# Optimization experiments

Measured on AMD Instinct MI355X. Metric: run time of the kernel, lower is better.

## Reference

```python
import jax, jax.numpy as jnp
import numpy as np

N = 50000   # query points
N2 = 50000  # key/value points
C = 128     # n_channels
G = 8       # n_groups
S = 16      # n_samples
CS = C // G # n_share_channels
EPS = 1e-5


def setup_inputs() -> dict:
    key = jax.random.key(0)
    ks = jax.random.split(key, 16)
    std = 0.02
    return {
        "p": jax.random.normal(ks[0], (N, 3), jnp.float32),
        "x": jax.random.normal(ks[1], (N, C), jnp.float32),
        "p2": jax.random.normal(ks[2], (N2, 3), jnp.float32),
        "x2": jax.random.normal(ks[3], (N2, C), jnp.float32),
        "idx": jax.random.randint(ks[4], (N, S), 0, N2, jnp.int32),
        "Wq": jax.random.normal(ks[5], (C, C), jnp.float32) * std,
        "bq": jnp.zeros((C,), jnp.float32),
        "Wk": jax.random.normal(ks[6], (C, C), jnp.float32) * std,
        "bk": jnp.zeros((C,), jnp.float32),
        "Wv": jax.random.normal(ks[7], (C, C), jnp.float32) * std,
        "bv": jnp.zeros((C,), jnp.float32),
        # linear_p: Conv1d(3,3,1) -> BN(3) -> ReLU -> Conv1d(3, 2G, 1)
        "W1": jax.random.normal(ks[8], (3, 3), jnp.float32) * 0.5,
        "b1": jnp.zeros((3,), jnp.float32),
        "bn_gamma": jnp.ones((3,), jnp.float32),
        "bn_beta": jnp.zeros((3,), jnp.float32),
        "bn_mean": jnp.zeros((3,), jnp.float32),
        "bn_var": jnp.ones((3,), jnp.float32),
        "W2": jax.random.normal(ks[9], (2 * G, 3), jnp.float32) * 0.5,
        "b2": jnp.zeros((2 * G,), jnp.float32),
    }


def reference(p, x, p2, x2, idx,
              Wq, bq, Wk, bk, Wv, bv,
              W1, b1, bn_gamma, bn_beta, bn_mean, bn_var, W2, b2):
    n = x.shape[0]
    # Q/K/V projections
    x_q = x @ Wq.T + bq                       # (n, C)
    x_k = (x2 @ Wk.T + bk)[idx]               # (n, S, C)  KNN gather
    x_v = (x2 @ Wv.T + bv)[idx]               # (n, S, C)
    # relative positions
    p_r = p2[idx] - p[:, None, :]             # (n, S, 3)
    # linear_p (pointwise convs == per-neighbor MLP over the 3 coord channels)
    h = p_r @ W1.T + b1
    h = (h - bn_mean) * jax.lax.rsqrt(bn_var + EPS) * bn_gamma + bn_beta
    h = jax.nn.relu(h)
    pe = h @ W2.T + b2                        # (n, S, 2G)
    p_rq, p_rk = jnp.split(pe, 2, axis=-1)    # each (n, S, G)
    # grouped attention
    k4 = x_k.reshape(n, S, G, CS) + p_rk[..., None]
    q4 = x_q.reshape(n, 1, G, CS) + p_rq[..., None]
    logits = jnp.sum(k4 * q4, axis=-1) / np.float32(np.sqrt(CS))  # (n, S, G)
    w = jax.nn.softmax(logits, axis=1)        # softmax over neighbors
    out = jnp.einsum('nsgc,nsg->ngc', x_v.reshape(n, S, G, CS), w)
    return out.reshape(n, C)
```

## Files before the change

kernel.cpp:

```cpp
#include <hip/hip_runtime.h>
#include <hip/hip_bf16.h>

#define NQ   50000
#define NKV  50000
#define CC   128
#define GG   8
#define SS   16
#define CSH  16

typedef short    bf16x8 __attribute__((ext_vector_type(8)));
typedef float    f32x4  __attribute__((ext_vector_type(4)));
typedef unsigned u32x4  __attribute__((ext_vector_type(4)));
typedef unsigned u32x2  __attribute__((ext_vector_type(2)));
typedef int      i32x4  __attribute__((ext_vector_type(4)));

__device__ __forceinline__ float bf_lo(unsigned u){ union{unsigned x; float f;} v; v.x = u << 16;        return v.f; }
__device__ __forceinline__ float bf_hi(unsigned u){ union{unsigned x; float f;} v; v.x = u & 0xffff0000u; return v.f; }
__device__ __forceinline__ unsigned short f2bfu(float f){
    __hip_bfloat16 h = __float2bfloat16(f);
    return *reinterpret_cast<unsigned short*>(&h);
}
__device__ __forceinline__ short f2bfs(float f){
    __hip_bfloat16 h = __float2bfloat16(f);
    return *reinterpret_cast<short*>(&h);
}

__device__ __forceinline__ void load16bf(const __hip_bfloat16* ptr, float* o){
    const u32x4* p4 = reinterpret_cast<const u32x4*>(ptr);
    u32x4 a = p4[0]; u32x4 b = p4[1];
    o[0]=bf_lo(a[0]);  o[1]=bf_hi(a[0]);  o[2]=bf_lo(a[1]);  o[3]=bf_hi(a[1]);
    o[4]=bf_lo(a[2]);  o[5]=bf_hi(a[2]);  o[6]=bf_lo(a[3]);  o[7]=bf_hi(a[3]);
    o[8]=bf_lo(b[0]);  o[9]=bf_hi(b[0]);  o[10]=bf_lo(b[1]); o[11]=bf_hi(b[1]);
    o[12]=bf_lo(b[2]); o[13]=bf_hi(b[2]); o[14]=bf_lo(b[3]); o[15]=bf_hi(b[3]);
}

__device__ __forceinline__ bf16x8 cvt8(const float* p){
    const f32x4* q = reinterpret_cast<const f32x4*>(p);
    f32x4 u = q[0], v = q[1];
    bf16x8 r;
    r[0]=f2bfs(u[0]); r[1]=f2bfs(u[1]); r[2]=f2bfs(u[2]); r[3]=f2bfs(u[3]);
    r[4]=f2bfs(v[0]); r[5]=f2bfs(v[1]); r[6]=f2bfs(v[2]); r[7]=f2bfs(v[3]);
    return r;
}

__global__ __launch_bounds__(256) void qkv_gemm(
    const float* __restrict__ x,
    const float* __restrict__ x2,
    const float* __restrict__ Wq, const float* __restrict__ Wk,
    const float* __restrict__ Wv,
    const float* __restrict__ bq, const float* __restrict__ bk,
    const float* __restrict__ bv,
    __hip_bfloat16* __restrict__ Qf,
    __hip_bfloat16* __restrict__ KVf)
{
    __shared__ short lds16[16384];

    const int tid  = threadIdx.x;
    const int wave = tid >> 6;
    const int lane = tid & 63;
    const int r    = lane & 15;
    const int kq   = lane >> 4;
    const int base = blockIdx.x * 128 + wave * 32;

    auto stageW = [&](const float* __restrict__ W){
        #pragma unroll
        for (int i = 0; i < 8; ++i) {
            const int o   = i * 2048 + tid * 8;
            const bf16x8 v = cvt8(W + o);
            const int row = o >> 7, col = o & 127;
            const int lchunk = (((row >> 4) * 4 + (col >> 5)) << 6)
                             + (((col >> 3) & 3) << 4) + (row & 15);
            *reinterpret_cast<bf16x8*>(&lds16[lchunk * 8]) = v;
        }
    };

    auto loadB = [&](const float* __restrict__ src, bf16x8 (&bfrag)[2][4]){
        #pragma unroll
        for (int mt = 0; mt < 2; ++mt) {
            int row = base + mt * 16 + r;
            if (row >= NQ) row = NQ - 1;
            const float* xr = src + (size_t)row * CC + kq * 8;
            #pragma unroll
            for (int kb = 0; kb < 4; ++kb)
                bfrag[mt][kb] = cvt8(xr + kb * 32);
        }
    };

    auto runTiles = [&](const bf16x8 (&bfrag)[2][4], const float* __restrict__ bias,
                        short* __restrict__ dstb, int dstride, int hoff){
        #pragma unroll
        for (int t = 0; t < 8; ++t) {
            bf16x8 af[4];
            #pragma unroll
            for (int kb = 0; kb < 4; ++kb)
                af[kb] = *reinterpret_cast<const bf16x8*>(
                    &lds16[(((t * 4 + kb) << 6) + lane) * 8]);

            f32x4 acc0 = {0.f,0.f,0.f,0.f}, acc1 = {0.f,0.f,0.f,0.f};
            #pragma unroll
            for (int kb = 0; kb < 4; ++kb) {
                acc0 = __builtin_amdgcn_mfma_f32_16x16x32_bf16(af[kb], bfrag[0][kb], acc0, 0, 0, 0);
                acc1 = __builtin_amdgcn_mfma_f32_16x16x32_bf16(af[kb], bfrag[1][kb], acc1, 0, 0, 0);
            }

            const f32x4 bi = *reinterpret_cast<const f32x4*>(bias + t * 16 + kq * 4);
            #pragma unroll
            for (int mt = 0; mt < 2; ++mt) {
                const int row = base + mt * 16 + r;
                if (row < NQ) {
                    const f32x4 a = mt ? acc1 : acc0;
                    u32x2 pk;
                    pk[0] = (unsigned)f2bfu(a[0] + bi[0]) | ((unsigned)f2bfu(a[1] + bi[1]) << 16);
                    pk[1] = (unsigned)f2bfu(a[2] + bi[2]) | ((unsigned)f2bfu(a[3] + bi[3]) << 16);
                    *reinterpret_cast<u32x2*>(
                        dstb + (size_t)row * dstride + hoff + t * 16 + kq * 4) = pk;
                }
            }
        }
    };

    bf16x8 fq[2][4], fkv[2][4];
    loadB(x,  fq);
    loadB(x2, fkv);

    stageW(Wq);
    __syncthreads();
    runTiles(fq, bq, (short*)Qf, CC, 0);
    __syncthreads();
    stageW(Wk);
    __syncthreads();
    runTiles(fkv, bk, (short*)KVf, 2 * CC, 0);
    __syncthreads();
    stageW(Wv);
    __syncthreads();
    runTiles(fkv, bv, (short*)KVf, 2 * CC, CC);
}

__global__ __launch_bounds__(256) void attn_kernel(
    const float* __restrict__ p,
    const float* __restrict__ p2,
    const int*   __restrict__ idx,
    const float* __restrict__ W1,
    const float* __restrict__ b1,
    const float* __restrict__ bn_gamma,
    const float* __restrict__ bn_beta,
    const float* __restrict__ bn_mean,
    const float* __restrict__ bn_var,
    const float* __restrict__ W2,
    const float* __restrict__ b2,
    const __hip_bfloat16* __restrict__ Qf,
    const __hip_bfloat16* __restrict__ KVf,
    float* __restrict__ out)
{
    const int tid = blockIdx.x * 256 + threadIdx.x;
    if (tid >= NQ * GG) return;
    const int n = tid >> 3;
    const int g = tid & 7;

    float fw1[3][3], fb1[3];
    #pragma unroll
    for (int j = 0; j < 3; ++j) {
        const float sc = bn_gamma[j] * rsqrtf(bn_var[j] + 1e-5f);
        #pragma unroll
        for (int k = 0; k < 3; ++k) fw1[j][k] = W1[j*3 + k] * sc;
        fb1[j] = (b1[j] - bn_mean[j]) * sc + bn_beta[j];
    }
    const float w2q0 = W2[g*3+0],     w2q1 = W2[g*3+1],     w2q2 = W2[g*3+2];
    const float w2k0 = W2[(g+8)*3+0], w2k1 = W2[(g+8)*3+1], w2k2 = W2[(g+8)*3+2];
    const float b2q = b2[g], b2k = b2[g+8];

    const float px = p[(size_t)n*3+0];
    const float py = p[(size_t)n*3+1];
    const float pz = p[(size_t)n*3+2];

    int nbr[SS];
    {
        const i32x4* ip = reinterpret_cast<const i32x4*>(idx + (size_t)n * SS);
        i32x4 i0 = ip[0], i1 = ip[1], i2 = ip[2], i3 = ip[3];
        nbr[0]=i0[0]; nbr[1]=i0[1]; nbr[2]=i0[2]; nbr[3]=i0[3];
        nbr[4]=i1[0]; nbr[5]=i1[1]; nbr[6]=i1[2]; nbr[7]=i1[3];
        nbr[8]=i2[0]; nbr[9]=i2[1]; nbr[10]=i2[2]; nbr[11]=i2[3];
        nbr[12]=i3[0]; nbr[13]=i3[1]; nbr[14]=i3[2]; nbr[15]=i3[3];
    }

    float q[CSH];
    load16bf(Qf + (size_t)n * CC + g * CSH, q);

    float acc[CSH];
    #pragma unroll
    for (int c = 0; c < CSH; ++c) acc[c] = 0.f;
    float sum = 0.f;
    float m = -3.0e38f;

    #pragma unroll 4
    for (int s = 0; s < SS; ++s) {
        const int i = nbr[s];
        const __hip_bfloat16* kv = KVf + (size_t)i * (2 * CC) + g * CSH;

        float kk[CSH], vv[CSH];
        load16bf(kv, kk);
        load16bf(kv + CC, vv);

        const float rx = p2[(size_t)i*3+0] - px;
        const float ry = p2[(size_t)i*3+1] - py;
        const float rz = p2[(size_t)i*3+2] - pz;
        const float h0 = fmaxf(fw1[0][0]*rx + fw1[0][1]*ry + fw1[0][2]*rz + fb1[0], 0.f);
        const float h1 = fmaxf(fw1[1][0]*rx + fw1[1][1]*ry + fw1[1][2]*rz + fb1[1], 0.f);
        const float h2 = fmaxf(fw1[2][0]*rx + fw1[2][1]*ry + fw1[2][2]*rz + fb1[2], 0.f);
        const float prq = w2q0*h0 + w2q1*h1 + w2q2*h2 + b2q;
        const float prk = w2k0*h0 + w2k1*h1 + w2k2*h2 + b2k;

        float d = 0.f;
        #pragma unroll
        for (int c = 0; c < CSH; ++c) d += (kk[c] + prk) * (q[c] + prq);
        d *= 0.25f;

        const float mnew = fmaxf(m, d);
        const float corr = __expf(m - mnew);
        const float w    = __expf(d - mnew);
        sum = sum * corr + w;
        #pragma unroll
        for (int c = 0; c < CSH; ++c) acc[c] = acc[c] * corr + w * vv[c];
        m = mnew;
    }

    const float inv = 1.f / sum;

    f32x4* op = reinterpret_cast<f32x4*>(out + (size_t)n * CC + g * CSH);
    f32x4 o0 = {acc[0]*inv,  acc[1]*inv,  acc[2]*inv,  acc[3]*inv};
    f32x4 o1 = {acc[4]*inv,  acc[5]*inv,  acc[6]*inv,  acc[7]*inv};
    f32x4 o2 = {acc[8]*inv,  acc[9]*inv,  acc[10]*inv, acc[11]*inv};
    f32x4 o3 = {acc[12]*inv, acc[13]*inv, acc[14]*inv, acc[15]*inv};
    op[0] = o0; op[1] = o1; op[2] = o2; op[3] = o3;
}

extern "C" void kernel_launch(void* const* d_in, const int* in_sizes, int n_in,
                              void* d_out, int out_size, void* d_ws, size_t ws_size,
                              hipStream_t stream) {
    const float* p   = (const float*)d_in[0];
    const float* x   = (const float*)d_in[1];
    const float* p2  = (const float*)d_in[2];
    const float* x2  = (const float*)d_in[3];
    const int*   idx = (const int*)d_in[4];
    const float* Wq  = (const float*)d_in[5];
    const float* bq  = (const float*)d_in[6];
    const float* Wk  = (const float*)d_in[7];
    const float* bk  = (const float*)d_in[8];
    const float* Wv  = (const float*)d_in[9];
    const float* bv  = (const float*)d_in[10];
    const float* W1  = (const float*)d_in[11];
    const float* b1  = (const float*)d_in[12];
    const float* bng = (const float*)d_in[13];
    const float* bnb = (const float*)d_in[14];
    const float* bnm = (const float*)d_in[15];
    const float* bnv = (const float*)d_in[16];
    const float* W2  = (const float*)d_in[17];
    const float* b2  = (const float*)d_in[18];
    float* out = (float*)d_out;

    __hip_bfloat16* Qf  = (__hip_bfloat16*)d_ws;
    __hip_bfloat16* KVf = Qf + (size_t)NQ * CC;

    qkv_gemm<<<dim3(391), 256, 0, stream>>>(
        x, x2, Wq, Wk, Wv, bq, bk, bv, Qf, KVf);

    const int nthreads = NQ * GG;
    attn_kernel<<<(nthreads + 255) / 256, 256, 0, stream>>>(
        p, p2, idx, W1, b1, bng, bnb, bnm, bnv, W2, b2, Qf, KVf, out);
}
```

Before: 212.6 us.

## Split QKV GEMM across grid.y and use two-pass softmax with algebraic dot expansion

The QKV projection kernel now launches a 391x3 grid, one projection per blockIdx.y, so it no longer serialises three weight stagings and tile passes inside each block. This adds parallelism at the cost of loading x2 twice. The attention kernel drops the online softmax. It first computes all 16 logits, expanding (k+prk)·(q+prq) into dot + prq*sumk + prk*sumq + 16*prk*prq, then does a max/exp/normalise pass, then gathers V in a separate loop. This removes the per-step rescaling of the accumulator, but raises register pressure and splits the K and V gathers into two phases.

```diff
diff --git a/kernel.cpp b/kernel.cpp
--- a/kernel.cpp
+++ b/kernel.cpp
@@ -61,79 +61,66 @@
     const int r    = lane & 15;
     const int kq   = lane >> 4;
     const int base = blockIdx.x * 128 + wave * 32;
-
-    auto stageW = [&](const float* __restrict__ W){
-        #pragma unroll
-        for (int i = 0; i < 8; ++i) {
-            const int o   = i * 2048 + tid * 8;
-            const bf16x8 v = cvt8(W + o);
-            const int row = o >> 7, col = o & 127;
-            const int lchunk = (((row >> 4) * 4 + (col >> 5)) << 6)
-                             + (((col >> 3) & 3) << 4) + (row & 15);
-            *reinterpret_cast<bf16x8*>(&lds16[lchunk * 8]) = v;
+    const int proj = blockIdx.y;
+
+    const float* src  = (proj == 0) ? x  : x2;
+    const float* W    = (proj == 0) ? Wq : (proj == 1 ? Wk : Wv);
+    const float* bias = (proj == 0) ? bq : (proj == 1 ? bk : bv);
+    short* dstb   = (proj == 0) ? (short*)Qf : (short*)KVf;
+    const int dstride = (proj == 0) ? CC : 2 * CC;
+    const int hoff    = (proj == 2) ? CC : 0;
+
+    bf16x8 bfrag[2][4];
+    #pragma unroll
+    for (int mt = 0; mt < 2; ++mt) {
+        int row = base + mt * 16 + r;
+        if (row >= NQ) row = NQ - 1;
+        const float* xr = src + (size_t)row * CC + kq * 8;
+        #pragma unroll
+        for (int kb = 0; kb < 4; ++kb)
+            bfrag[mt][kb] = cvt8(xr + kb * 32);
+    }
+
+    #pragma unroll
+    for (int i = 0; i < 8; ++i) {
+        const int o   = i * 2048 + tid * 8;
+        const bf16x8 v = cvt8(W + o);
+        const int row = o >> 7, col = o & 127;
+        const int lchunk = (((row >> 4) * 4 + (col >> 5)) << 6)
+                         + (((col >> 3) & 3) << 4) + (row & 15);
+        *reinterpret_cast<bf16x8*>(&lds16[lchunk * 8]) = v;
+    }
+    __syncthreads();
+
+    #pragma unroll
+    for (int t = 0; t < 8; ++t) {
+        bf16x8 af[4];
+        #pragma unroll
+        for (int kb = 0; kb < 4; ++kb)
+            af[kb] = *reinterpret_cast<const bf16x8*>(
+                &lds16[(((t * 4 + kb) << 6) + lane) * 8]);
+
+        f32x4 acc0 = {0.f,0.f,0.f,0.f}, acc1 = {0.f,0.f,0.f,0.f};
+        #pragma unroll
+        for (int kb = 0; kb < 4; ++kb) {
+            acc0 = __builtin_amdgcn_mfma_f32_16x16x32_bf16(af[kb], bfrag[0][kb], acc0, 0, 0, 0);
+            acc1 = __builtin_amdgcn_mfma_f32_16x16x32_bf16(af[kb], bfrag[1][kb], acc1, 0, 0, 0);
         }
-    };
-
-    auto loadB = [&](const float* __restrict__ src, bf16x8 (&bfrag)[2][4]){
+
+        const f32x4 bi = *reinterpret_cast<const f32x4*>(bias + t * 16 + kq * 4);
         #pragma unroll
         for (int mt = 0; mt < 2; ++mt) {
-            int row = base + mt * 16 + r;
-            if (row >= NQ) row = NQ - 1;
-            const float* xr = src + (size_t)row * CC + kq * 8;
-            #pragma unroll
-            for (int kb = 0; kb < 4; ++kb)
-                bfrag[mt][kb] = cvt8(xr + kb * 32);
-        }
-    };
-
-    auto runTiles = [&](const bf16x8 (&bfrag)[2][4], const float* __restrict__ bias,
-                        short* __restrict__ dstb, int dstride, int hoff){
-        #pragma unroll
-        for (int t = 0; t < 8; ++t) {
-            bf16x8 af[4];
-            #pragma unroll
-            for (int kb = 0; kb < 4; ++kb)
-                af[kb] = *reinterpret_cast<const bf16x8*>(
-                    &lds16[(((t * 4 + kb) << 6) + lane) * 8]);
-
-            f32x4 acc0 = {0.f,0.f,0.f,0.f}, acc1 = {0.f,0.f,0.f,0.f};
-            #pragma unroll
-            for (int kb = 0; kb < 4; ++kb) {
-                acc0 = __builtin_amdgcn_mfma_f32_16x16x32_bf16(af[kb], bfrag[0][kb], acc0, 0, 0, 0);
-                acc1 = __builtin_amdgcn_mfma_f32_16x16x32_bf16(af[kb], bfrag[1][kb], acc1, 0, 0, 0);
-            }
-
-            const f32x4 bi = *reinterpret_cast<const f32x4*>(bias + t * 16 + kq * 4);
-            #pragma unroll
-            for (int mt = 0; mt < 2; ++mt) {
-                const int row = base + mt * 16 + r;
-                if (row < NQ) {
-                    const f32x4 a = mt ? acc1 : acc0;
-                    u32x2 pk;
-                    pk[0] = (unsigned)f2bfu(a[0] + bi[0]) | ((unsigned)f2bfu(a[1] + bi[1]) << 16);
-                    pk[1] = (unsigned)f2bfu(a[2] + bi[2]) | ((unsigned)f2bfu(a[3] + bi[3]) << 16);
-                    *reinterpret_cast<u32x2*>(
-                        dstb + (size_t)row * dstride + hoff + t * 16 + kq * 4) = pk;
-                }
+            const int row = base + mt * 16 + r;
+            if (row < NQ) {
+                const f32x4 a = mt ? acc1 : acc0;
+                u32x2 pk;
+                pk[0] = (unsigned)f2bfu(a[0] + bi[0]) | ((unsigned)f2bfu(a[1] + bi[1]) << 16);
+                pk[1] = (unsigned)f2bfu(a[2] + bi[2]) | ((unsigned)f2bfu(a[3] + bi[3]) << 16);
+                *reinterpret_cast<u32x2*>(
+                    dstb + (size_t)row * dstride + hoff + t * 16 + kq * 4) = pk;
             }
         }
-    };
-
-    bf16x8 fq[2][4], fkv[2][4];
-    loadB(x,  fq);
-    loadB(x2, fkv);
-
-    stageW(Wq);
-    __syncthreads();
-    runTiles(fq, bq, (short*)Qf, CC, 0);
-    __syncthreads();
-    stageW(Wk);
-    __syncthreads();
-    runTiles(fkv, bk, (short*)KVf, 2 * CC, 0);
-    __syncthreads();
-    stageW(Wv);
-    __syncthreads();
-    runTiles(fkv, bv, (short*)KVf, 2 * CC, CC);
+    }
 }
 
 __global__ __launch_bounds__(256) void attn_kernel(
@@ -185,21 +172,16 @@
 
     float q[CSH];
     load16bf(Qf + (size_t)n * CC + g * CSH, q);
-
-    float acc[CSH];
-    #pragma unroll
-    for (int c = 0; c < CSH; ++c) acc[c] = 0.f;
-    float sum = 0.f;
-    float m = -3.0e38f;
-
-    #pragma unroll 4
+    float sumq = 0.f;
+    #pragma unroll
+    for (int c = 0; c < CSH; ++c) sumq += q[c];
+
+    float d[SS];
+    #pragma unroll
     for (int s = 0; s < SS; ++s) {
         const int i = nbr[s];
-        const __hip_bfloat16* kv = KVf + (size_t)i * (2 * CC) + g * CSH;
-
-        float kk[CSH], vv[CSH];
-        load16bf(kv, kk);
-        load16bf(kv + CC, vv);
+        float kk[CSH];
+        load16bf(KVf + (size_t)i * (2 * CC) + g * CSH, kk);
 
         const float rx = p2[(size_t)i*3+0] - px;
         const float ry = p2[(size_t)i*3+1] - py;
@@ -210,27 +192,39 @@
         const float prq = w2q0*h0 + w2q1*h1 + w2q2*h2 + b2q;
         const float prk = w2k0*h0 + w2k1*h1 + w2k2*h2 + b2k;
 
-        float d = 0.f;
-        #pragma unroll
-        for (int c = 0; c < CSH; ++c) d += (kk[c] + prk) * (q[c] + prq);
-        d *= 0.25f;
-
-        const float mnew = fmaxf(m, d);
-        const float corr = __expf(m - mnew);
-        const float w    = __expf(d - mnew);
-        sum = sum * corr + w;
-        #pragma unroll
-        for (int c = 0; c < CSH; ++c) acc[c] = acc[c] * corr + w * vv[c];
-        m = mnew;
-    }
-
+        float dot = 0.f, sumk = 0.f;
+        #pragma unroll
+        for (int c = 0; c < CSH; ++c) { dot += kk[c]*q[c]; sumk += kk[c]; }
+        d[s] = (dot + prq*sumk + prk*sumq + 16.f*prk*prq) * 0.25f;
+    }
+
+    float m = d[0];
+    #pragma unroll
+    for (int s = 1; s < SS; ++s) m = fmaxf(m, d[s]);
+    float w[SS], sum = 0.f;
+    #pragma unroll
+    for (int s = 0; s < SS; ++s) { w[s] = __expf(d[s] - m); sum += w[s]; }
     const float inv = 1.f / sum;
+    #pragma unroll
+    for (int s = 0; s < SS; ++s) w[s] *= inv;
+
+    float acc[CSH];
+    #pragma unroll
+    for (int c = 0; c < CSH; ++c) acc[c] = 0.f;
+    #pragma unroll
+    for (int s = 0; s < SS; ++s) {
+        const int i = nbr[s];
+        float vv[CSH];
+        load16bf(KVf + (size_t)i * (2 * CC) + CC + g * CSH, vv);
+        #pragma unroll
+        for (int c = 0; c < CSH; ++c) acc[c] += w[s] * vv[c];
+    }
 
     f32x4* op = reinterpret_cast<f32x4*>(out + (size_t)n * CC + g * CSH);
-    f32x4 o0 = {acc[0]*inv,  acc[1]*inv,  acc[2]*inv,  acc[3]*inv};
-    f32x4 o1 = {acc[4]*inv,  acc[5]*inv,  acc[6]*inv,  acc[7]*inv};
-    f32x4 o2 = {acc[8]*inv,  acc[9]*inv,  acc[10]*inv, acc[11]*inv};
-    f32x4 o3 = {acc[12]*inv, acc[13]*inv, acc[14]*inv, acc[15]*inv};
+    f32x4 o0 = {acc[0],  acc[1],  acc[2],  acc[3]};
+    f32x4 o1 = {acc[4],  acc[5],  acc[6],  acc[7]};
+    f32x4 o2 = {acc[8],  acc[9],  acc[10], acc[11]};
+    f32x4 o3 = {acc[12], acc[13], acc[14], acc[15]};
     op[0] = o0; op[1] = o1; op[2] = o2; op[3] = o3;
 }
 
@@ -261,7 +255,7 @@
     __hip_bfloat16* Qf  = (__hip_bfloat16*)d_ws;
     __hip_bfloat16* KVf = Qf + (size_t)NQ * CC;
 
-    qkv_gemm<<<dim3(391), 256, 0, stream>>>(
+    qkv_gemm<<<dim3(391, 3), 256, 0, stream>>>(
         x, x2, Wq, Wk, Wv, bq, bk, bv, Qf, KVf);
 
     const int nthreads = NQ * GG;
```

Result: slower. 227.5 us (+7.0%).

## Pre-convert QKV weights to bf16 LDS layout and split projections across grid

Applied to the files above, without the earlier changes.

A small prep kernel now converts Wq/Wk/Wv to bf16 once, already in the LDS tile order. The GEMM kernel takes a second grid dimension so each block handles one projection, and copies its weight tile with global_load_lds direct-to-LDS loads. This removes the repeated per-block fp32-to-bf16 weight conversion and the serialized stage/sync phases, and triples the block count for more parallelism. The cost is an extra kernel launch, and x2 rows are read twice, once by the K block and once by the V block.

```diff
diff --git a/kernel.cpp b/kernel.cpp
--- a/kernel.cpp
+++ b/kernel.cpp
@@ -43,11 +43,30 @@
     return r;
 }
 
+__global__ __launch_bounds__(256) void wprep(
+    const float* __restrict__ Wq, const float* __restrict__ Wk,
+    const float* __restrict__ Wv,
+    __hip_bfloat16* __restrict__ Wp)
+{
+    const float* W = (blockIdx.x == 0) ? Wq : (blockIdx.x == 1) ? Wk : Wv;
+    __hip_bfloat16* o = Wp + blockIdx.x * 16384;
+    #pragma unroll
+    for (int k = 0; k < 8; ++k) {
+        const int chunk = k * 256 + threadIdx.x;
+        const int q   = chunk >> 6;
+        const int rem = chunk & 63;
+        const int c3  = rem >> 4, r15 = rem & 15;
+        const int row  = ((q >> 2) << 4) | r15;
+        const int colb = ((q & 3) << 5) | (c3 << 3);
+        const bf16x8 v = cvt8(W + row * 128 + colb);
+        *reinterpret_cast<bf16x8*>(o + chunk * 8) = v;
+    }
+}
+
 __global__ __launch_bounds__(256) void qkv_gemm(
     const float* __restrict__ x,
     const float* __restrict__ x2,
-    const float* __restrict__ Wq, const float* __restrict__ Wk,
-    const float* __restrict__ Wv,
+    const __hip_bfloat16* __restrict__ Wp,
     const float* __restrict__ bq, const float* __restrict__ bk,
     const float* __restrict__ bv,
     __hip_bfloat16* __restrict__ Qf,
@@ -61,79 +80,67 @@
     const int r    = lane & 15;
     const int kq   = lane >> 4;
     const int base = blockIdx.x * 128 + wave * 32;
-
-    auto stageW = [&](const float* __restrict__ W){
+    const int proj = blockIdx.y;
+
+    const float* src  = (proj == 0) ? x  : x2;
+    const float* bias = (proj == 0) ? bq : (proj == 1 ? bk : bv);
+    short* dstb   = (proj == 0) ? (short*)Qf : (short*)KVf;
+    const int dstride = (proj == 0) ? CC : 2 * CC;
+    const int hoff    = (proj == 2) ? CC : 0;
+
+    {
+        const __hip_bfloat16* Wsrc = Wp + proj * 16384;
         #pragma unroll
         for (int i = 0; i < 8; ++i) {
-            const int o   = i * 2048 + tid * 8;
-            const bf16x8 v = cvt8(W + o);
-            const int row = o >> 7, col = o & 127;
-            const int lchunk = (((row >> 4) * 4 + (col >> 5)) << 6)
-                             + (((col >> 3) & 3) << 4) + (row & 15);
-            *reinterpret_cast<bf16x8*>(&lds16[lchunk * 8]) = v;
+            const int el = i * 2048 + wave * 512;
+            __builtin_amdgcn_global_load_lds(
+                (const __attribute__((address_space(1))) void*)(Wsrc + el + lane * 8),
+                (__attribute__((address_space(3))) void*)(&lds16[el]),
+                16, 0, 0);
         }
-    };
-
-    auto loadB = [&](const float* __restrict__ src, bf16x8 (&bfrag)[2][4]){
+    }
+
+    bf16x8 bfrag[2][4];
+    #pragma unroll
+    for (int mt = 0; mt < 2; ++mt) {
+        int row = base + mt * 16 + r;
+        if (row >= NQ) row = NQ - 1;
+        const float* xr = src + (size_t)row * CC + kq * 8;
+        #pragma unroll
+        for (int kb = 0; kb < 4; ++kb)
+            bfrag[mt][kb] = cvt8(xr + kb * 32);
+    }
+    __syncthreads();
+
+    #pragma unroll
+    for (int t = 0; t < 8; ++t) {
+        bf16x8 af[4];
+        #pragma unroll
+        for (int kb = 0; kb < 4; ++kb)
+            af[kb] = *reinterpret_cast<const bf16x8*>(
+                &lds16[(((t * 4 + kb) << 6) + lane) * 8]);
+
+        f32x4 acc0 = {0.f,0.f,0.f,0.f}, acc1 = {0.f,0.f,0.f,0.f};
+        #pragma unroll
+        for (int kb = 0; kb < 4; ++kb) {
+            acc0 = __builtin_amdgcn_mfma_f32_16x16x32_bf16(af[kb], bfrag[0][kb], acc0, 0, 0, 0);
+            acc1 = __builtin_amdgcn_mfma_f32_16x16x32_bf16(af[kb], bfrag[1][kb], acc1, 0, 0, 0);
+        }
+
+        const f32x4 bi = *reinterpret_cast<const f32x4*>(bias + t * 16 + kq * 4);
         #pragma unroll
         for (int mt = 0; mt < 2; ++mt) {
-            int row = base + mt * 16 + r;
-            if (row >= NQ) row = NQ - 1;
-            const float* xr = src + (size_t)row * CC + kq * 8;
-            #pragma unroll
-            for (int kb = 0; kb < 4; ++kb)
-                bfrag[mt][kb] = cvt8(xr + kb * 32);
-        }
-    };
-
-    auto runTiles = [&](const bf16x8 (&bfrag)[2][4], const float* __restrict__ bias,
-                        short* __restrict__ dstb, int dstride, int hoff){
-        #pragma unroll
-        for (int t = 0; t < 8; ++t) {
-            bf16x8 af[4];
-            #pragma unroll
-            for (int kb = 0; kb < 4; ++kb)
-                af[kb] = *reinterpret_cast<const bf16x8*>(
-                    &lds16[(((t * 4 + kb) << 6) + lane) * 8]);
-
-            f32x4 acc0 = {0.f,0.f,0.f,0.f}, acc1 = {0.f,0.f,0.f,0.f};
-            #pragma unroll
-            for (int kb = 0; kb < 4; ++kb) {
-                acc0 = __builtin_amdgcn_mfma_f32_16x16x32_bf16(af[kb], bfrag[0][kb], acc0, 0, 0, 0);
-                acc1 = __builtin_amdgcn_mfma_f32_16x16x32_bf16(af[kb], bfrag[1][kb], acc1, 0, 0, 0);
-            }
-
-            const f32x4 bi = *reinterpret_cast<const f32x4*>(bias + t * 16 + kq * 4);
-            #pragma unroll
-            for (int mt = 0; mt < 2; ++mt) {
-                const int row = base + mt * 16 + r;
-                if (row < NQ) {
-                    const f32x4 a = mt ? acc1 : acc0;
-                    u32x2 pk;
-                    pk[0] = (unsigned)f2bfu(a[0] + bi[0]) | ((unsigned)f2bfu(a[1] + bi[1]) << 16);
-                    pk[1] = (unsigned)f2bfu(a[2] + bi[2]) | ((unsigned)f2bfu(a[3] + bi[3]) << 16);
-                    *reinterpret_cast<u32x2*>(
-                        dstb + (size_t)row * dstride + hoff + t * 16 + kq * 4) = pk;
-                }
+            const int row = base + mt * 16 + r;
+            if (row < NQ) {
+                const f32x4 a = mt ? acc1 : acc0;
+                u32x2 pk;
+                pk[0] = (unsigned)f2bfu(a[0] + bi[0]) | ((unsigned)f2bfu(a[1] + bi[1]) << 16);
+                pk[1] = (unsigned)f2bfu(a[2] + bi[2]) | ((unsigned)f2bfu(a[3] + bi[3]) << 16);
+                *reinterpret_cast<u32x2*>(
+                    dstb + (size_t)row * dstride + hoff + t * 16 + kq * 4) = pk;
             }
         }
-    };
-
-    bf16x8 fq[2][4], fkv[2][4];
-    loadB(x,  fq);
-    loadB(x2, fkv);
-
-    stageW(Wq);
-    __syncthreads();
-    runTiles(fq, bq, (short*)Qf, CC, 0);
-    __syncthreads();
-    stageW(Wk);
-    __syncthreads();
-    runTiles(fkv, bk, (short*)KVf, 2 * CC, 0);
-    __syncthreads();
-    stageW(Wv);
-    __syncthreads();
-    runTiles(fkv, bv, (short*)KVf, 2 * CC, CC);
+    }
 }
 
 __global__ __launch_bounds__(256) void attn_kernel(
@@ -258,13 +265,15 @@
     const float* b2  = (const float*)d_in[18];
     float* out = (float*)d_out;
 
-    __hip_bfloat16* Qf  = (__hip_bfloat16*)d_ws;
+    __hip_bfloat16* Wp  = (__hip_bfloat16*)d_ws;
+    __hip_bfloat16* Qf  = Wp + 3 * 16384;
     __hip_bfloat16* KVf = Qf + (size_t)NQ * CC;
 
-    qkv_gemm<<<dim3(391), 256, 0, stream>>>(
-        x, x2, Wq, Wk, Wv, bq, bk, bv, Qf, KVf);
-
-    const int nthreads = NQ * GG;
-    attn_kernel<<<(nthreads + 255) / 256, 256, 0, stream>>>(
+    wprep<<<3, 256, 0, stream>>>(Wq, Wk, Wv, Wp);
+
+    qkv_gemm<<<dim3(391, 3), 256, 0, stream>>>(
+        x, x2, Wp, bq, bk, bv, Qf, KVf);
+
+    attn_kernel<<<(NQ * GG + 255) / 256, 256, 0, stream>>>(
         p, p2, idx, W1, b1, bng, bnb, bnm, bnv, W2, b2, Qf, KVf, out);
 }
```

New measurement: 211.0 us. About the same (-0.8%).

## Split QKV projection across a second grid dimension, one projection per block

Applied to the files above, without the earlier changes.

The QKV GEMM kernel now launches a 391x3 grid where blockIdx.y selects the Q, K or V projection, instead of each block computing all three in sequence. This removes the serialized stage-weight/sync/compute phases inside one block and gives three times as many blocks to fill the 256 CUs. The cost is that the x2 tile is loaded and converted twice (once each for the K and V blocks), which adds redundant global reads.

```diff
diff --git a/kernel.cpp b/kernel.cpp
--- a/kernel.cpp
+++ b/kernel.cpp
@@ -61,79 +61,66 @@
     const int r    = lane & 15;
     const int kq   = lane >> 4;
     const int base = blockIdx.x * 128 + wave * 32;
-
-    auto stageW = [&](const float* __restrict__ W){
-        #pragma unroll
-        for (int i = 0; i < 8; ++i) {
-            const int o   = i * 2048 + tid * 8;
-            const bf16x8 v = cvt8(W + o);
-            const int row = o >> 7, col = o & 127;
-            const int lchunk = (((row >> 4) * 4 + (col >> 5)) << 6)
-                             + (((col >> 3) & 3) << 4) + (row & 15);
-            *reinterpret_cast<bf16x8*>(&lds16[lchunk * 8]) = v;
+    const int proj = blockIdx.y;
+
+    const float* src  = (proj == 0) ? x  : x2;
+    const float* W    = (proj == 0) ? Wq : (proj == 1 ? Wk : Wv);
+    const float* bias = (proj == 0) ? bq : (proj == 1 ? bk : bv);
+    short* dstb   = (proj == 0) ? (short*)Qf : (short*)KVf;
+    const int dstride = (proj == 0) ? CC : 2 * CC;
+    const int hoff    = (proj == 2) ? CC : 0;
+
+    bf16x8 bfrag[2][4];
+    #pragma unroll
+    for (int mt = 0; mt < 2; ++mt) {
+        int row = base + mt * 16 + r;
+        if (row >= NQ) row = NQ - 1;
+        const float* xr = src + (size_t)row * CC + kq * 8;
+        #pragma unroll
+        for (int kb = 0; kb < 4; ++kb)
+            bfrag[mt][kb] = cvt8(xr + kb * 32);
+    }
+
+    #pragma unroll
+    for (int i = 0; i < 8; ++i) {
+        const int o   = i * 2048 + tid * 8;
+        const bf16x8 v = cvt8(W + o);
+        const int row = o >> 7, col = o & 127;
+        const int lchunk = (((row >> 4) * 4 + (col >> 5)) << 6)
+                         + (((col >> 3) & 3) << 4) + (row & 15);
+        *reinterpret_cast<bf16x8*>(&lds16[lchunk * 8]) = v;
+    }
+    __syncthreads();
+
+    #pragma unroll
+    for (int t = 0; t < 8; ++t) {
+        bf16x8 af[4];
+        #pragma unroll
+        for (int kb = 0; kb < 4; ++kb)
+            af[kb] = *reinterpret_cast<const bf16x8*>(
+                &lds16[(((t * 4 + kb) << 6) + lane) * 8]);
+
+        f32x4 acc0 = {0.f,0.f,0.f,0.f}, acc1 = {0.f,0.f,0.f,0.f};
+        #pragma unroll
+        for (int kb = 0; kb < 4; ++kb) {
+            acc0 = __builtin_amdgcn_mfma_f32_16x16x32_bf16(af[kb], bfrag[0][kb], acc0, 0, 0, 0);
+            acc1 = __builtin_amdgcn_mfma_f32_16x16x32_bf16(af[kb], bfrag[1][kb], acc1, 0, 0, 0);
         }
-    };
-
-    auto loadB = [&](const float* __restrict__ src, bf16x8 (&bfrag)[2][4]){
+
+        const f32x4 bi = *reinterpret_cast<const f32x4*>(bias + t * 16 + kq * 4);
         #pragma unroll
         for (int mt = 0; mt < 2; ++mt) {
-            int row = base + mt * 16 + r;
-            if (row >= NQ) row = NQ - 1;
-            const float* xr = src + (size_t)row * CC + kq * 8;
-            #pragma unroll
-            for (int kb = 0; kb < 4; ++kb)
-                bfrag[mt][kb] = cvt8(xr + kb * 32);
-        }
-    };
-
-    auto runTiles = [&](const bf16x8 (&bfrag)[2][4], const float* __restrict__ bias,
-                        short* __restrict__ dstb, int dstride, int hoff){
-        #pragma unroll
-        for (int t = 0; t < 8; ++t) {
-            bf16x8 af[4];
-            #pragma unroll
-            for (int kb = 0; kb < 4; ++kb)
-                af[kb] = *reinterpret_cast<const bf16x8*>(
-                    &lds16[(((t * 4 + kb) << 6) + lane) * 8]);
-
-            f32x4 acc0 = {0.f,0.f,0.f,0.f}, acc1 = {0.f,0.f,0.f,0.f};
-            #pragma unroll
-            for (int kb = 0; kb < 4; ++kb) {
-                acc0 = __builtin_amdgcn_mfma_f32_16x16x32_bf16(af[kb], bfrag[0][kb], acc0, 0, 0, 0);
-                acc1 = __builtin_amdgcn_mfma_f32_16x16x32_bf16(af[kb], bfrag[1][kb], acc1, 0, 0, 0);
-            }
-
-            const f32x4 bi = *reinterpret_cast<const f32x4*>(bias + t * 16 + kq * 4);
-            #pragma unroll
-            for (int mt = 0; mt < 2; ++mt) {
-                const int row = base + mt * 16 + r;
-                if (row < NQ) {
-                    const f32x4 a = mt ? acc1 : acc0;
-                    u32x2 pk;
-                    pk[0] = (unsigned)f2bfu(a[0] + bi[0]) | ((unsigned)f2bfu(a[1] + bi[1]) << 16);
-                    pk[1] = (unsigned)f2bfu(a[2] + bi[2]) | ((unsigned)f2bfu(a[3] + bi[3]) << 16);
-                    *reinterpret_cast<u32x2*>(
-                        dstb + (size_t)row * dstride + hoff + t * 16 + kq * 4) = pk;
-                }
+            const int row = base + mt * 16 + r;
+            if (row < NQ) {
+                const f32x4 a = mt ? acc1 : acc0;
+                u32x2 pk;
+                pk[0] = (unsigned)f2bfu(a[0] + bi[0]) | ((unsigned)f2bfu(a[1] + bi[1]) << 16);
+                pk[1] = (unsigned)f2bfu(a[2] + bi[2]) | ((unsigned)f2bfu(a[3] + bi[3]) << 16);
+                *reinterpret_cast<u32x2*>(
+                    dstb + (size_t)row * dstride + hoff + t * 16 + kq * 4) = pk;
             }
         }
-    };
-
-    bf16x8 fq[2][4], fkv[2][4];
-    loadB(x,  fq);
-    loadB(x2, fkv);
-
-    stageW(Wq);
-    __syncthreads();
-    runTiles(fq, bq, (short*)Qf, CC, 0);
-    __syncthreads();
-    stageW(Wk);
-    __syncthreads();
-    runTiles(fkv, bk, (short*)KVf, 2 * CC, 0);
-    __syncthreads();
-    stageW(Wv);
-    __syncthreads();
-    runTiles(fkv, bv, (short*)KVf, 2 * CC, CC);
+    }
 }
 
 __global__ __launch_bounds__(256) void attn_kernel(
@@ -261,10 +248,9 @@
     __hip_bfloat16* Qf  = (__hip_bfloat16*)d_ws;
     __hip_bfloat16* KVf = Qf + (size_t)NQ * CC;
 
-    qkv_gemm<<<dim3(391), 256, 0, stream>>>(
+    qkv_gemm<<<dim3(391, 3), 256, 0, stream>>>(
         x, x2, Wq, Wk, Wv, bq, bk, bv, Qf, KVf);
 
-    const int nthreads = NQ * GG;
-    attn_kernel<<<(nthreads + 255) / 256, 256, 0, stream>>>(
+    attn_kernel<<<(NQ * GG + 255) / 256, 256, 0, stream>>>(
         p, p2, idx, W1, b1, bng, bnb, bnm, bnv, W2, b2, Qf, KVf, out);
 }
```

Result: faster. 207.8 us (-2.3%).
